# Kernel tuning notes

Measured on AMD Instinct MI355X. Metric: run time of the kernel, lower is better.

## Reference

```python
import jax, jax.numpy as jnp
import numpy as np

AFWD = 0.999
EPS = 1e-05


def setup_inputs() -> dict:
    key = jax.random.key(0)
    N, L = 8192, 4096
    x = jax.random.normal(key, (N, L), dtype=jnp.float32)
    m = jnp.zeros((L,), dtype=jnp.float32)    # EMA mean buffer (init 0)
    var = jnp.ones((L,), dtype=jnp.float32)   # EMA var buffer (init 1)
    return {"x": x, "m": m, "var": var}


def reference(x, m, var):
    """Online-normalization forward: sequential scan over the N (row) dim,
    vectorized over the L feature dim. Matches ControlNormalization.forward."""
    afwd = AFWD

    def step(carry, xt):
        mu, v = carry                      # each [L]
        scale = jnp.sqrt(v + EPS)
        d = xt - mu
        out = d / scale
        v_new = afwd * v + afwd * (1.0 - afwd) * d * d
        mu_new = mu + (1.0 - afwd) * d
        return (mu_new, v_new), out

    _, out = jax.lax.scan(step, (m, var), x)  # out: [N, L]
    return out
```

## Files before the change

### kernel.cpp

```cpp
#include <hip/hip_runtime.h>
#include <math.h>

#define AFWD 0.999f
#define ONE_MINUS_A (1.0f - 0.999f)
#define KCOEF (0.999f * (1.0f - 0.999f))
#define EPSV 1e-5f

typedef float floatx4 __attribute__((ext_vector_type(4)));

__global__ __launch_bounds__(256) void
passA(const float* __restrict__ x, float* __restrict__ Bmu,
      float* __restrict__ See, float* __restrict__ Te, int L4, int CH) {
  int idx  = blockIdx.x * blockDim.x + threadIdx.x;
  int col4 = idx % L4;
  int c    = idx / L4;
  const floatx4* xv = (const floatx4*)x;
  int base = c * CH * L4 + col4;

  float mu[4] = {0.f, 0.f, 0.f, 0.f};
  float s[4]  = {0.f, 0.f, 0.f, 0.f};
  float t[4]  = {0.f, 0.f, 0.f, 0.f};
#pragma unroll 4
  for (int i = 0; i < CH; ++i) {
    floatx4 v = xv[base + i * L4];
#pragma unroll
    for (int k = 0; k < 4; ++k) {
      float e = v[k] - mu[k];
      s[k] = fmaf(AFWD, s[k], e * e);
      t[k] += e;
      mu[k] = fmaf(ONE_MINUS_A, e, mu[k]);
    }
  }
  int o = c * L4 + col4;
  floatx4 om = {mu[0], mu[1], mu[2], mu[3]};
  floatx4 os = {s[0], s[1], s[2], s[3]};
  floatx4 ot = {t[0], t[1], t[2], t[3]};
  ((floatx4*)Bmu)[o] = om;
  ((floatx4*)See)[o] = os;
  ((floatx4*)Te)[o]  = ot;
}

__global__ __launch_bounds__(256) void
passBfused(const float* __restrict__ m, const float* __restrict__ var,
           const float* __restrict__ Bmu, const float* __restrict__ See,
           const float* __restrict__ Te, float* __restrict__ Ms,
           float* __restrict__ Vs, int L, int SUB, int GS,
           float A, float c_eg, float Sgg, float G,
           float Asup, float c_sup, float Sggsup) {
  __shared__ float Bs[8][32], Ss[8][32], Ts[8][32];
  __shared__ float MgL[8][32], VgL[8][32];

  int g  = threadIdx.x >> 5;
  int lc = threadIdx.x & 31;
  int l  = blockIdx.x * 32 + lc;

  {
    int base = g * SUB * L + l;
    float B = 0.f, T = 0.f, S = 0.f;
#pragma unroll 4
    for (int k = 0; k < SUB; ++k) {
      int o = base + k * L;
      float b2 = Bmu[o];
      float s2 = See[o];
      float t2 = Te[o];
      S = fmaf(A, S, fmaf(Sgg * B, B, fmaf(-2.0f * c_eg * B, t2, s2)));
      T = fmaf(-G, B, T + t2);
      B = fmaf(A, B, b2);
    }
    Bs[g][lc] = B;
    Ss[g][lc] = S;
    Ts[g][lc] = T;
  }

  __syncthreads();

  if (threadIdx.x < 32) {
    float M = m[l];
    float V = var[l];
#pragma unroll
    for (int gg = 0; gg < 8; ++gg) {
      if (gg >= GS) break;
      MgL[gg][lc] = M;
      VgL[gg][lc] = V;
      float b = Bs[gg][lc];
      float s = Ss[gg][lc];
      float t = Ts[gg][lc];
      float sum = fmaf(M * M, Sggsup, fmaf(-2.0f * c_sup * M, t, s));
      V = fmaf(Asup, V, KCOEF * sum);
      M = fmaf(Asup, M, b);
    }
  }

  __syncthreads();

  {
    float M = MgL[g][lc];
    float V = VgL[g][lc];
    int base = g * SUB * L + l;
#pragma unroll 4
    for (int k = 0; k < SUB; ++k) {
      int o = base + k * L;
      Ms[o] = M;
      Vs[o] = V;
      float b = Bmu[o];
      float s = See[o];
      float t = Te[o];
      float sum = fmaf(M * M, Sgg, fmaf(-2.0f * c_eg * M, t, s));
      V = fmaf(A, V, KCOEF * sum);
      M = fmaf(A, M, b);
    }
  }
}

__global__ __launch_bounds__(256) void
passC(const float* __restrict__ x, const float* __restrict__ Ms,
      const float* __restrict__ Vs, float* __restrict__ out, int L4, int CH) {
  int idx  = blockIdx.x * blockDim.x + threadIdx.x;
  int col4 = idx % L4;
  int c    = idx / L4;
  const floatx4* xv = (const floatx4*)x;
  floatx4* ov = (floatx4*)out;
  int base = c * CH * L4 + col4;

  int o = c * L4 + col4;
  floatx4 m4 = ((const floatx4*)Ms)[o];
  floatx4 v4 = ((const floatx4*)Vs)[o];
  float mu[4] = {m4[0], m4[1], m4[2], m4[3]};
  float vv[4] = {v4[0], v4[1], v4[2], v4[3]};
#pragma unroll 4
  for (int i = 0; i < CH; ++i) {
    floatx4 v = xv[base + i * L4];
    floatx4 oe;
#pragma unroll
    for (int k = 0; k < 4; ++k) {
      float d = v[k] - mu[k];
      oe[k] = d * rsqrtf(vv[k] + EPSV);
      vv[k] = fmaf(AFWD, vv[k], KCOEF * (d * d));
      mu[k] = fmaf(ONE_MINUS_A, d, mu[k]);
    }
    __builtin_nontemporal_store(oe, &ov[base + i * L4]);
  }
}

extern "C" void kernel_launch(void* const* d_in, const int* in_sizes, int n_in,
                              void* d_out, int out_size, void* d_ws, size_t ws_size,
                              hipStream_t stream) {
  const float* x   = (const float*)d_in[0];
  const float* m   = (const float*)d_in[1];
  const float* var = (const float*)d_in[2];
  float* out = (float*)d_out;

  int L  = in_sizes[1];
  int N  = in_sizes[0] / L;
  int L4 = L / 4;

  int C = 128;
  while (C > 1 &&
         ((size_t)5 * C * L * sizeof(float) > ws_size || (N % C) != 0))
    C >>= 1;
  int CH = N / C;
  int SUB = (C >= 16) ? 16 : C;
  int GS  = C / SUB;

  double a = 0.999;
  float A    = (float)pow(a, (double)CH);
  float c_eg = (float)pow(a, (double)(CH - 1));
  float Sgg  = (float)(pow(a, (double)(CH - 1)) * (1.0 - pow(a, (double)CH)) / (1.0 - a));
  float G    = (float)((1.0 - pow(a, (double)CH)) / (1.0 - a));
  double nS = (double)SUB * CH;
  float Asup   = (float)pow(a, nS);
  float c_sup  = (float)pow(a, nS - 1.0);
  float Sggsup = (float)(pow(a, nS - 1.0) * (1.0 - pow(a, nS)) / (1.0 - a));

  float* ws  = (float*)d_ws;
  size_t CL  = (size_t)C * L;
  float* Bmu  = ws;
  float* See  = ws + CL;
  float* Te   = ws + 2 * CL;
  float* Ms   = ws + 3 * CL;
  float* Vs   = ws + 4 * CL;

  int gridBlocks = (C * L4) / 256;
  passA<<<gridBlocks, 256, 0, stream>>>(x, Bmu, See, Te, L4, CH);
  passBfused<<<L / 32, 256, 0, stream>>>(m, var, Bmu, See, Te, Ms, Vs, L,
                                         SUB, GS, A, c_eg, Sgg, G,
                                         Asup, c_sup, Sggsup);
  passC<<<gridBlocks, 256, 0, stream>>>(x, Ms, Vs, out, L4, CH);
}
```

Before: 74.54 us.

## Split feature columns into halves and overlap passC of one half with passA of other

The column dimension is split in two halves, and the three-pass chunked scan becomes a five-launch pipeline. A combined kernel runs the output pass for the first half alongside the chunk-summary pass for the second half, so the two bandwidth-heavy passes share the device. This targets the idle time and tail effects between dependent launches, at the cost of more launches and smaller per-launch grids for the edge stages.

```diff
diff --git a/kernel.cpp b/kernel.cpp
--- a/kernel.cpp
+++ b/kernel.cpp
@@ -8,12 +8,13 @@
 
 typedef float floatx4 __attribute__((ext_vector_type(4)));
 
-__global__ __launch_bounds__(256) void
-passA(const float* __restrict__ x, float* __restrict__ Bmu,
-      float* __restrict__ See, float* __restrict__ Te, int L4, int CH) {
-  int idx  = blockIdx.x * blockDim.x + threadIdx.x;
-  int col4 = idx % L4;
-  int c    = idx / L4;
+
+__device__ __forceinline__ void
+passA_body(const float* __restrict__ x, float* __restrict__ Bmu,
+           float* __restrict__ See, float* __restrict__ Te,
+           int L4, int L4h, int CH, int colOff, int ih) {
+  int col4 = colOff + (ih % L4h);
+  int c    = ih / L4h;
   const floatx4* xv = (const floatx4*)x;
   int base = c * CH * L4 + col4;
 
@@ -40,11 +41,71 @@
   ((floatx4*)Te)[o]  = ot;
 }
 
+__device__ __forceinline__ void
+passC_body(const float* __restrict__ x, const float* __restrict__ Ms,
+           const float* __restrict__ Vs, float* __restrict__ out,
+           int L4, int L4h, int CH, int colOff, int ih) {
+  int col4 = colOff + (ih % L4h);
+  int c    = ih / L4h;
+  const floatx4* xv = (const floatx4*)x;
+  floatx4* ov = (floatx4*)out;
+  int base = c * CH * L4 + col4;
+
+  int o = c * L4 + col4;
+  floatx4 m4 = ((const floatx4*)Ms)[o];
+  floatx4 v4 = ((const floatx4*)Vs)[o];
+  float mu[4] = {m4[0], m4[1], m4[2], m4[3]};
+  float vv[4] = {v4[0], v4[1], v4[2], v4[3]};
+#pragma unroll 4
+  for (int i = 0; i < CH; ++i) {
+    floatx4 v = xv[base + i * L4];
+    floatx4 oe;
+#pragma unroll
+    for (int k = 0; k < 4; ++k) {
+      float d = v[k] - mu[k];
+      oe[k] = d * rsqrtf(vv[k] + EPSV);
+      vv[k] = fmaf(AFWD, vv[k], KCOEF * (d * d));
+      mu[k] = fmaf(ONE_MINUS_A, d, mu[k]);
+    }
+    __builtin_nontemporal_store(oe, &ov[base + i * L4]);
+  }
+}
+
+__global__ __launch_bounds__(256) void
+kA(const float* __restrict__ x, float* __restrict__ Bmu,
+   float* __restrict__ See, float* __restrict__ Te,
+   int L4, int L4h, int CH, int colOff) {
+  passA_body(x, Bmu, See, Te, L4, L4h, CH, colOff,
+             blockIdx.x * 256 + threadIdx.x);
+}
+
+__global__ __launch_bounds__(256) void
+kC(const float* __restrict__ x, const float* __restrict__ Ms,
+   const float* __restrict__ Vs, float* __restrict__ out,
+   int L4, int L4h, int CH, int colOff) {
+  passC_body(x, Ms, Vs, out, L4, L4h, CH, colOff,
+             blockIdx.x * 256 + threadIdx.x);
+}
+
+__global__ __launch_bounds__(256) void
+kCA(const float* __restrict__ x, const float* __restrict__ Ms,
+    const float* __restrict__ Vs, float* __restrict__ out,
+    float* __restrict__ Bmu, float* __restrict__ See, float* __restrict__ Te,
+    int L4, int L4h, int CH, int HB) {
+  if ((int)blockIdx.x < HB) {
+    passC_body(x, Ms, Vs, out, L4, L4h, CH, 0,
+               blockIdx.x * 256 + threadIdx.x);
+  } else {
+    passA_body(x, Bmu, See, Te, L4, L4h, CH, L4h,
+               (blockIdx.x - HB) * 256 + threadIdx.x);
+  }
+}
+
 __global__ __launch_bounds__(256) void
 passBfused(const float* __restrict__ m, const float* __restrict__ var,
            const float* __restrict__ Bmu, const float* __restrict__ See,
            const float* __restrict__ Te, float* __restrict__ Ms,
-           float* __restrict__ Vs, int L, int SUB, int GS,
+           float* __restrict__ Vs, int L, int SUB, int GS, int colBase,
            float A, float c_eg, float Sgg, float G,
            float Asup, float c_sup, float Sggsup) {
   __shared__ float Bs[8][32], Ss[8][32], Ts[8][32];
@@ -52,7 +113,7 @@
 
   int g  = threadIdx.x >> 5;
   int lc = threadIdx.x & 31;
-  int l  = blockIdx.x * 32 + lc;
+  int l  = colBase + blockIdx.x * 32 + lc;
 
   {
     int base = g * SUB * L + l;
@@ -112,36 +173,6 @@
   }
 }
 
-__global__ __launch_bounds__(256) void
-passC(const float* __restrict__ x, const float* __restrict__ Ms,
-      const float* __restrict__ Vs, float* __restrict__ out, int L4, int CH) {
-  int idx  = blockIdx.x * blockDim.x + threadIdx.x;
-  int col4 = idx % L4;
-  int c    = idx / L4;
-  const floatx4* xv = (const floatx4*)x;
-  floatx4* ov = (floatx4*)out;
-  int base = c * CH * L4 + col4;
-
-  int o = c * L4 + col4;
-  floatx4 m4 = ((const floatx4*)Ms)[o];
-  floatx4 v4 = ((const floatx4*)Vs)[o];
-  float mu[4] = {m4[0], m4[1], m4[2], m4[3]};
-  float vv[4] = {v4[0], v4[1], v4[2], v4[3]};
-#pragma unroll 4
-  for (int i = 0; i < CH; ++i) {
-    floatx4 v = xv[base + i * L4];
-    floatx4 oe;
-#pragma unroll
-    for (int k = 0; k < 4; ++k) {
-      float d = v[k] - mu[k];
-      oe[k] = d * rsqrtf(vv[k] + EPSV);
-      vv[k] = fmaf(AFWD, vv[k], KCOEF * (d * d));
-      mu[k] = fmaf(ONE_MINUS_A, d, mu[k]);
-    }
-    __builtin_nontemporal_store(oe, &ov[base + i * L4]);
-  }
-}
-
 extern "C" void kernel_launch(void* const* d_in, const int* in_sizes, int n_in,
                               void* d_out, int out_size, void* d_ws, size_t ws_size,
                               hipStream_t stream) {
@@ -153,6 +184,8 @@
   int L  = in_sizes[1];
   int N  = in_sizes[0] / L;
   int L4 = L / 4;
+  int L4h = L4 / 2;
+  int Lh  = L / 2;
 
   int C = 128;
   while (C > 1 &&
@@ -174,16 +207,21 @@
 
   float* ws  = (float*)d_ws;
   size_t CL  = (size_t)C * L;
-  float* Bmu  = ws;
-  float* See  = ws + CL;
-  float* Te   = ws + 2 * CL;
-  float* Ms   = ws + 3 * CL;
-  float* Vs   = ws + 4 * CL;
-
-  int gridBlocks = (C * L4) / 256;
-  passA<<<gridBlocks, 256, 0, stream>>>(x, Bmu, See, Te, L4, CH);
-  passBfused<<<L / 32, 256, 0, stream>>>(m, var, Bmu, See, Te, Ms, Vs, L,
-                                         SUB, GS, A, c_eg, Sgg, G,
-                                         Asup, c_sup, Sggsup);
-  passC<<<gridBlocks, 256, 0, stream>>>(x, Ms, Vs, out, L4, CH);
-}
+  float* Bmu = ws;
+  float* See = ws + CL;
+  float* Te  = ws + 2 * CL;
+  float* Ms  = ws + 3 * CL;
+  float* Vs  = ws + 4 * CL;
+
+  int HB = (C * L4h) / 256;
+  int BB = Lh / 32;
+
+  kA<<<HB, 256, 0, stream>>>(x, Bmu, See, Te, L4, L4h, CH, 0);
+  passBfused<<<BB, 256, 0, stream>>>(m, var, Bmu, See, Te, Ms, Vs, L, SUB, GS,
+                                     0, A, c_eg, Sgg, G, Asup, c_sup, Sggsup);
+  kCA<<<2 * HB, 256, 0, stream>>>(x, Ms, Vs, out, Bmu, See, Te, L4, L4h, CH,
+                                  HB);
+  passBfused<<<BB, 256, 0, stream>>>(m, var, Bmu, See, Te, Ms, Vs, L, SUB, GS,
+                                     Lh, A, c_eg, Sgg, G, Asup, c_sup, Sggsup);
+  kC<<<HB, 256, 0, stream>>>(x, Ms, Vs, out, L4, L4h, CH, L4h);
+}
```

New measurement: 86.01 us. +15.4%, slower.

## Fuse three-pass chunked scan into one per-column-stripe kernel with shared-memory carries

Applied to the files above, without the earlier changes.

Replaces the three kernels (chunk summaries, carry propagation, output pass) with a single kernel where each block owns a 16-column stripe and computes chunk summaries, the carry scan, and outputs using shared memory. This removes the workspace writes/reads and two kernel launches. In exchange, each row access per block is only 64 contiguous bytes, grid is limited to L/16 blocks, and the serial carry phase idles most threads between memory-bound phases.

```diff
diff --git a/kernel.cpp b/kernel.cpp
--- a/kernel.cpp
+++ b/kernel.cpp
@@ -8,137 +8,133 @@
 
 typedef float floatx4 __attribute__((ext_vector_type(4)));
 
-__global__ __launch_bounds__(256) void
-passA(const float* __restrict__ x, float* __restrict__ Bmu,
-      float* __restrict__ See, float* __restrict__ Te, int L4, int CH) {
-  int idx  = blockIdx.x * blockDim.x + threadIdx.x;
-  int col4 = idx % L4;
-  int c    = idx / L4;
+#define TPB   512
+#define BCOLS 16
+#define BC4   4
+#define MAXSUB 128
+
+__global__ __launch_bounds__(TPB) void
+stripe_cn(const float* __restrict__ x, const float* __restrict__ m,
+          const float* __restrict__ var, float* __restrict__ out,
+          int L4, int CH, int SUBS, int GSUP,
+          float A, float c_eg, float Sgg, float G,
+          float Asup, float c_sup, float Sggsup) {
+  __shared__ float sB[MAXSUB][BCOLS], sS[MAXSUB][BCOLS], sT[MAXSUB][BCOLS];
+  __shared__ float sM[MAXSUB][BCOLS], sV[MAXSUB][BCOLS];
+  __shared__ float gB[8][BCOLS], gS[8][BCOLS], gT[8][BCOLS];
+  __shared__ float gM[8][BCOLS], gV[8][BCOLS];
+
+  int tid  = threadIdx.x;
+  int c4   = tid & (BC4 - 1);
+  int sub  = tid >> 2;
+  int col4 = blockIdx.x * BC4 + c4;
   const floatx4* xv = (const floatx4*)x;
-  int base = c * CH * L4 + col4;
+  int base = sub * CH * L4 + col4;
+  bool active = (sub < SUBS);
 
-  float mu[4] = {0.f, 0.f, 0.f, 0.f};
-  float s[4]  = {0.f, 0.f, 0.f, 0.f};
-  float t[4]  = {0.f, 0.f, 0.f, 0.f};
+  if (active) {
+    float mu[4] = {0.f, 0.f, 0.f, 0.f};
+    float sv[4] = {0.f, 0.f, 0.f, 0.f};
+    float tv[4] = {0.f, 0.f, 0.f, 0.f};
 #pragma unroll 4
-  for (int i = 0; i < CH; ++i) {
-    floatx4 v = xv[base + i * L4];
+    for (int i = 0; i < CH; ++i) {
+      floatx4 v = xv[base + i * L4];
+#pragma unroll
+      for (int k = 0; k < 4; ++k) {
+        float e = v[k] - mu[k];
+        sv[k] = fmaf(AFWD, sv[k], e * e);
+        tv[k] += e;
+        mu[k] = fmaf(ONE_MINUS_A, e, mu[k]);
+      }
+    }
 #pragma unroll
     for (int k = 0; k < 4; ++k) {
-      float e = v[k] - mu[k];
-      s[k] = fmaf(AFWD, s[k], e * e);
-      t[k] += e;
-      mu[k] = fmaf(ONE_MINUS_A, e, mu[k]);
+      sB[sub][c4 * 4 + k] = mu[k];
+      sS[sub][c4 * 4 + k] = sv[k];
+      sT[sub][c4 * 4 + k] = tv[k];
     }
   }
-  int o = c * L4 + col4;
-  floatx4 om = {mu[0], mu[1], mu[2], mu[3]};
-  floatx4 os = {s[0], s[1], s[2], s[3]};
-  floatx4 ot = {t[0], t[1], t[2], t[3]};
-  ((floatx4*)Bmu)[o] = om;
-  ((floatx4*)See)[o] = os;
-  ((floatx4*)Te)[o]  = ot;
-}
+  __syncthreads();
 
-__global__ __launch_bounds__(256) void
-passBfused(const float* __restrict__ m, const float* __restrict__ var,
-           const float* __restrict__ Bmu, const float* __restrict__ See,
-           const float* __restrict__ Te, float* __restrict__ Ms,
-           float* __restrict__ Vs, int L, int SUB, int GS,
-           float A, float c_eg, float Sgg, float G,
-           float Asup, float c_sup, float Sggsup) {
-  __shared__ float Bs[8][32], Ss[8][32], Ts[8][32];
-  __shared__ float MgL[8][32], VgL[8][32];
-
-  int g  = threadIdx.x >> 5;
-  int lc = threadIdx.x & 31;
-  int l  = blockIdx.x * 32 + lc;
-
-  {
-    int base = g * SUB * L + l;
+  if (tid < GSUP * BCOLS) {
+    int col = tid & (BCOLS - 1);
+    int g   = tid / BCOLS;
     float B = 0.f, T = 0.f, S = 0.f;
 #pragma unroll 4
-    for (int k = 0; k < SUB; ++k) {
-      int o = base + k * L;
-      float b2 = Bmu[o];
-      float s2 = See[o];
-      float t2 = Te[o];
+    for (int k = 0; k < 16; ++k) {
+      int su = g * 16 + k;
+      float b2 = sB[su][col];
+      float s2 = sS[su][col];
+      float t2 = sT[su][col];
       S = fmaf(A, S, fmaf(Sgg * B, B, fmaf(-2.0f * c_eg * B, t2, s2)));
       T = fmaf(-G, B, T + t2);
       B = fmaf(A, B, b2);
     }
-    Bs[g][lc] = B;
-    Ss[g][lc] = S;
-    Ts[g][lc] = T;
+    gB[g][col] = B;
+    gS[g][col] = S;
+    gT[g][col] = T;
   }
-
   __syncthreads();
 
-  if (threadIdx.x < 32) {
+  if (tid < BCOLS) {
+    int col = tid;
+    int l = blockIdx.x * BCOLS + col;
     float M = m[l];
     float V = var[l];
-#pragma unroll
-    for (int gg = 0; gg < 8; ++gg) {
-      if (gg >= GS) break;
-      MgL[gg][lc] = M;
-      VgL[gg][lc] = V;
-      float b = Bs[gg][lc];
-      float s = Ss[gg][lc];
-      float t = Ts[gg][lc];
+    for (int g = 0; g < GSUP; ++g) {
+      gM[g][col] = M;
+      gV[g][col] = V;
+      float b = gB[g][col];
+      float s = gS[g][col];
+      float t = gT[g][col];
       float sum = fmaf(M * M, Sggsup, fmaf(-2.0f * c_sup * M, t, s));
       V = fmaf(Asup, V, KCOEF * sum);
       M = fmaf(Asup, M, b);
     }
   }
-
   __syncthreads();
 
-  {
-    float M = MgL[g][lc];
-    float V = VgL[g][lc];
-    int base = g * SUB * L + l;
+  if (tid < GSUP * BCOLS) {
+    int col = tid & (BCOLS - 1);
+    int g   = tid / BCOLS;
+    float M = gM[g][col];
+    float V = gV[g][col];
 #pragma unroll 4
-    for (int k = 0; k < SUB; ++k) {
-      int o = base + k * L;
-      Ms[o] = M;
-      Vs[o] = V;
-      float b = Bmu[o];
-      float s = See[o];
-      float t = Te[o];
+    for (int k = 0; k < 16; ++k) {
+      int su = g * 16 + k;
+      sM[su][col] = M;
+      sV[su][col] = V;
+      float b = sB[su][col];
+      float s = sS[su][col];
+      float t = sT[su][col];
       float sum = fmaf(M * M, Sgg, fmaf(-2.0f * c_eg * M, t, s));
       V = fmaf(A, V, KCOEF * sum);
       M = fmaf(A, M, b);
     }
   }
-}
+  __syncthreads();
 
-__global__ __launch_bounds__(256) void
-passC(const float* __restrict__ x, const float* __restrict__ Ms,
-      const float* __restrict__ Vs, float* __restrict__ out, int L4, int CH) {
-  int idx  = blockIdx.x * blockDim.x + threadIdx.x;
-  int col4 = idx % L4;
-  int c    = idx / L4;
-  const floatx4* xv = (const floatx4*)x;
-  floatx4* ov = (floatx4*)out;
-  int base = c * CH * L4 + col4;
-
-  int o = c * L4 + col4;
-  floatx4 m4 = ((const floatx4*)Ms)[o];
-  floatx4 v4 = ((const floatx4*)Vs)[o];
-  float mu[4] = {m4[0], m4[1], m4[2], m4[3]};
-  float vv[4] = {v4[0], v4[1], v4[2], v4[3]};
-#pragma unroll 4
-  for (int i = 0; i < CH; ++i) {
-    floatx4 v = xv[base + i * L4];
-    floatx4 oe;
+  if (active) {
+    floatx4* ov = (floatx4*)out;
+    float M[4], V[4];
 #pragma unroll
     for (int k = 0; k < 4; ++k) {
-      float d = v[k] - mu[k];
-      oe[k] = d * rsqrtf(vv[k] + EPSV);
-      vv[k] = fmaf(AFWD, vv[k], KCOEF * (d * d));
-      mu[k] = fmaf(ONE_MINUS_A, d, mu[k]);
+      M[k] = sM[sub][c4 * 4 + k];
+      V[k] = sV[sub][c4 * 4 + k];
     }
-    __builtin_nontemporal_store(oe, &ov[base + i * L4]);
+#pragma unroll 4
+    for (int i = 0; i < CH; ++i) {
+      floatx4 v = xv[base + i * L4];
+      floatx4 oe;
+#pragma unroll
+      for (int k = 0; k < 4; ++k) {
+        float d = v[k] - M[k];
+        oe[k] = d * rsqrtf(V[k] + EPSV);
+        V[k] = fmaf(AFWD, V[k], KCOEF * (d * d));
+        M[k] = fmaf(ONE_MINUS_A, d, M[k]);
+      }
+      __builtin_nontemporal_store(oe, &ov[base + i * L4]);
+    }
   }
 }
 
@@ -154,36 +150,22 @@
   int N  = in_sizes[0] / L;
   int L4 = L / 4;
 
-  int C = 128;
-  while (C > 1 &&
-         ((size_t)5 * C * L * sizeof(float) > ws_size || (N % C) != 0))
-    C >>= 1;
-  int CH = N / C;
-  int SUB = (C >= 16) ? 16 : C;
-  int GS  = C / SUB;
+  int SUBS = MAXSUB;
+  while (SUBS > 16 && (N % SUBS) != 0) SUBS >>= 1;
+  int CH   = N / SUBS;
+  int GSUP = SUBS / 16;
 
   double a = 0.999;
   float A    = (float)pow(a, (double)CH);
   float c_eg = (float)pow(a, (double)(CH - 1));
   float Sgg  = (float)(pow(a, (double)(CH - 1)) * (1.0 - pow(a, (double)CH)) / (1.0 - a));
   float G    = (float)((1.0 - pow(a, (double)CH)) / (1.0 - a));
-  double nS = (double)SUB * CH;
+  double nS = 16.0 * CH;
   float Asup   = (float)pow(a, nS);
   float c_sup  = (float)pow(a, nS - 1.0);
   float Sggsup = (float)(pow(a, nS - 1.0) * (1.0 - pow(a, nS)) / (1.0 - a));
 
-  float* ws  = (float*)d_ws;
-  size_t CL  = (size_t)C * L;
-  float* Bmu  = ws;
-  float* See  = ws + CL;
-  float* Te   = ws + 2 * CL;
-  float* Ms   = ws + 3 * CL;
-  float* Vs   = ws + 4 * CL;
-
-  int gridBlocks = (C * L4) / 256;
-  passA<<<gridBlocks, 256, 0, stream>>>(x, Bmu, See, Te, L4, CH);
-  passBfused<<<L / 32, 256, 0, stream>>>(m, var, Bmu, See, Te, Ms, Vs, L,
-                                         SUB, GS, A, c_eg, Sgg, G,
-                                         Asup, c_sup, Sggsup);
-  passC<<<gridBlocks, 256, 0, stream>>>(x, Ms, Vs, out, L4, CH);
+  int blocks = L4 / BC4;
+  stripe_cn<<<blocks, TPB, 0, stream>>>(x, m, var, out, L4, CH, SUBS, GSUP,
+                                        A, c_eg, Sgg, G, Asup, c_sup, Sggsup);
 }
```

Measured after the change: 106.8 us. +43.3%, slower.
